# Optimization experiments

Hardware: AMD Instinct MI355X
Metric: run time of the kernel (lower is better)

## Reference

```python
import jax, jax.numpy as jnp
from jax import lax
import numpy as np

GRID, IMG, BLOCK = 60, 960, 16
BN_EPS = 1e-5


def _conv(x, w, b):
    return lax.conv_general_dilated(x, w, (1, 1), 'SAME', dimension_numbers=('NCHW', 'OIHW', 'NCHW')) + b[None, :, None, None]


def _bn(x, g, b):
    # inference BatchNorm with running_mean=0, running_var=1
    s = g * np.float32(1.0 / np.sqrt(1.0 + BN_EPS))
    return x * s[None, :, None, None] + b[None, :, None, None]


def _mlp(x, w1, b1, w2, b2):
    return jax.nn.relu(x @ w1.T + b1) @ w2.T + b2


def _lstm_layer(x, wih, whh, b):
    # x: [B,T,D]; torch gate order i,f,g,o; zero initial state
    B = x.shape[0]
    H = whh.shape[1]
    pre = jnp.swapaxes(x, 0, 1) @ wih.T + b  # [T,B,4H]

    def step(carry, p):
        h, c = carry
        z = p + h @ whh.T
        i, f, g, o = jnp.split(z, 4, axis=-1)
        c = jax.nn.sigmoid(f) * c + jax.nn.sigmoid(i) * jnp.tanh(g)
        h = jax.nn.sigmoid(o) * jnp.tanh(c)
        return (h, c), h

    z0 = jnp.zeros((B, H), x.dtype)
    (h, c), ys = lax.scan(step, (z0, z0), pre)
    return jnp.swapaxes(ys, 0, 1), h, c


def _forward(motion_vectors, boxes, track_ids, conv1_w, conv1_b, bn1_g, bn1_b, conv2_w, conv2_b, bn2_g, bn2_b, conv3_w, conv3_b, bn3_g, bn3_b, agg_w1, agg_b1, agg_w2, agg_b2, bx_w1, bx_b1, bx_w2, bx_b2, id_table, proj_w, proj_b, empty_slot, l0_wih, l0_whh, l0_b, l1_wih, l1_whh, l1_b, hb_w1, hb_b1, hb_w2, hb_b2, hc_w1, hc_b1, hc_w2, hc_b2, ht_w1, ht_b1, ht_w2, ht_b2):
    B = motion_vectors.shape[0]
    # ---- grid encoder (Conv-BN-ReLU x3) ----
    x = jax.nn.relu(_bn(_conv(motion_vectors, conv1_w, conv1_b), bn1_g, bn1_b))
    x = jax.nn.relu(_bn(_conv(x, conv2_w, conv2_b), bn2_g, bn2_b))
    gf = jax.nn.relu(_bn(_conv(x, conv3_w, conv3_b), bn3_g, bn3_b))  # [B,64,60,60]
    global_feat = gf.mean((-2, -1))  # AdaptiveAvgPool2d(1) -> [B,64]

    # ---- per-box motion statistics (vectorized masked reductions) ----
    bg = jnp.clip(boxes * (IMG / BLOCK), 0.0, GRID - 1e-6)  # grid coords
    ix1 = jnp.floor(bg[..., 0]); iy1 = jnp.floor(bg[..., 1])
    ix2 = jnp.maximum(ix1 + 1.0, jnp.ceil(bg[..., 2]))
    iy2 = jnp.maximum(iy1 + 1.0, jnp.ceil(bg[..., 3]))
    g = jnp.arange(GRID, dtype=bg.dtype)
    mx_ = (g >= ix1[..., None]) & (g < ix2[..., None])  # [B,N,60]
    my_ = (g >= iy1[..., None]) & (g < iy2[..., None])
    mask = my_[..., :, None] & mx_[..., None, :]  # [B,N,60,60]
    m = mask.astype(bg.dtype)
    cnt = m.sum((-2, -1))[..., None]  # [B,N,1], >= 1 by construction
    mv = motion_vectors  # [B,2,60,60]
    s1 = jnp.einsum('bnyx,bcyx->bnc', m, mv)
    s2 = jnp.einsum('bnyx,bcyx->bnc', m, mv * mv)
    mean = s1 / cnt
    var = (s2 - cnt * mean * mean) / jnp.maximum(cnt - 1.0, 1.0)  # unbiased, like torch .std()
    var_safe = jnp.where(cnt > 1.0, jnp.maximum(var, 1e-12), 1.0)
    std = jnp.where(cnt > 1.0, jnp.sqrt(var_safe), 0.0)
    BIG = jnp.asarray(1e9, bg.dtype)
    mn = jnp.min(jnp.where(mask[:, :, None], mv[:, None], BIG), axis=(-2, -1))   # [B,N,2]
    mx = jnp.max(jnp.where(mask[:, :, None], mv[:, None], -BIG), axis=(-2, -1))  # [B,N,2]
    stats = jnp.stack([mean[..., 0], mean[..., 1], std[..., 0], std[..., 1], mn[..., 0], mx[..., 0], mn[..., 1], mx[..., 1]], -1)  # [B,N,8]
    motion_emb = _mlp(stats, agg_w1, agg_b1, agg_w2, agg_b2)  # [B,N,64]

    # ---- slot initialization ----
    box_emb = _mlp(boxes, bx_w1, bx_b1, bx_w2, bx_b2)  # [B,N,64]
    id_emb = id_table[jnp.clip(track_ids, 0, 999)]  # [B,N,32]
    obj = jnp.concatenate([box_emb, id_emb, motion_emb], -1)  # [B,N,160]
    slots = obj @ proj_w.T + proj_b  # [B,300,128]; N == max_slots so no empty slots used

    # ---- 2-layer LSTM over the 300 slots (batch_first, eval -> no dropout) ----
    Ns = slots.shape[1]
    gexp = jnp.broadcast_to(global_feat[:, None, :], (B, Ns, global_feat.shape[-1]))
    lstm_in = jnp.concatenate([slots, gexp], -1)  # [B,300,192]
    y, h0, c0 = _lstm_layer(lstm_in, l0_wih, l0_whh, l0_b)
    y, h1, c1 = _lstm_layer(y, l1_wih, l1_whh, l1_b)  # [B,300,128]

    # ---- RT-DETR style heads ----
    pred_boxes = jax.nn.sigmoid(_mlp(y, hb_w1, hb_b1, hb_w2, hb_b2))  # [B,300,4]
    cls_logits = _mlp(y, hc_w1, hc_b1, hc_w2, hc_b2)  # [B,300,2]
    tid_logits = _mlp(y, ht_w1, ht_b1, ht_w2, ht_b2)  # [B,300,1000]
    h = jnp.stack([h0, h1])
    c = jnp.stack([c0, c1])
    return pred_boxes, cls_logits, tid_logits, h, c


def setup_inputs() -> dict:
    B, N = 32, 300
    key = jax.random.key(0)
    ks = iter(jax.random.split(key, 60))

    def w(*s):
        return jax.random.normal(next(ks), s, jnp.float32) * 0.05

    mv = jax.random.normal(next(ks), (B, 2, GRID, GRID), jnp.float32)
    bb = jax.random.uniform(next(ks), (B, N, 4), jnp.float32)
    boxes = jnp.concatenate([jnp.minimum(bb[..., :2], bb[..., 2:]), jnp.maximum(bb[..., :2], bb[..., 2:])], -1)
    track_ids = jax.random.randint(next(ks), (B, N), 0, 1000)
    return dict(
        motion_vectors=mv, boxes=boxes, track_ids=track_ids,
        conv1_w=w(32, 2, 3, 3), conv1_b=w(32), bn1_g=1.0 + w(32), bn1_b=w(32),
        conv2_w=w(64, 32, 3, 3), conv2_b=w(64), bn2_g=1.0 + w(64), bn2_b=w(64),
        conv3_w=w(64, 64, 3, 3), conv3_b=w(64), bn3_g=1.0 + w(64), bn3_b=w(64),
        agg_w1=w(32, 8), agg_b1=w(32), agg_w2=w(64, 32), agg_b2=w(64),
        bx_w1=w(32, 4), bx_b1=w(32), bx_w2=w(64, 32), bx_b2=w(64),
        id_table=w(1000, 32).at[0].set(0.0),
        proj_w=w(128, 160), proj_b=w(128), empty_slot=w(128),
        l0_wih=w(512, 192), l0_whh=w(512, 128), l0_b=w(512),
        l1_wih=w(512, 128), l1_whh=w(512, 128), l1_b=w(512),
        hb_w1=w(256, 128), hb_b1=w(256), hb_w2=w(4, 256), hb_b2=w(4),
        hc_w1=w(256, 128), hc_b1=w(256), hc_w2=w(2, 256), hc_b2=w(2),
        ht_w1=w(256, 128), ht_b1=w(256), ht_w2=w(1000, 256), ht_b2=w(1000))


def reference(motion_vectors, boxes, track_ids, conv1_w, conv1_b, bn1_g, bn1_b, conv2_w, conv2_b, bn2_g, bn2_b, conv3_w, conv3_b, bn3_g, bn3_b, agg_w1, agg_b1, agg_w2, agg_b2, bx_w1, bx_b1, bx_w2, bx_b2, id_table, proj_w, proj_b, empty_slot, l0_wih, l0_whh, l0_b, l1_wih, l1_whh, l1_b, hb_w1, hb_b1, hb_w2, hb_b2, hc_w1, hc_b1, hc_w2, hc_b2, ht_w1, ht_b1, ht_w2, ht_b2):
    return _forward(motion_vectors, boxes, track_ids, conv1_w, conv1_b, bn1_g, bn1_b, conv2_w, conv2_b, bn2_g, bn2_b, conv3_w, conv3_b, bn3_g, bn3_b, agg_w1, agg_b1, agg_w2, agg_b2, bx_w1, bx_b1, bx_w2, bx_b2, id_table, proj_w, proj_b, empty_slot, l0_wih, l0_whh, l0_b, l1_wih, l1_whh, l1_b, hb_w1, hb_b1, hb_w2, hb_b2, hc_w1, hc_b1, hc_w2, hc_b2, ht_w1, ht_b1, ht_w2, ht_b2)
```

## Files before the change

### kernel.cpp

```cpp
#include <hip/hip_runtime.h>
#include <hip/hip_bf16.h>
#include <math.h>

typedef unsigned short ushort_t;
typedef __attribute__((ext_vector_type(8))) short bf16x8;
typedef __attribute__((ext_vector_type(4))) float f32x4;

#define LOG2E 1.4426950408889634f

__device__ __forceinline__ float sigf(float x) {
  x = fminf(fmaxf(x, -30.f), 30.f);
  return 1.f / (1.f + __expf(-x));
}
__device__ __forceinline__ ushort_t f2bf(float x) {
  unsigned int b = __float_as_uint(x);
  unsigned int lsb = (b >> 16) & 1u;
  b += 0x7fffu + lsb;
  return (ushort_t)(b >> 16);
}
__device__ __forceinline__ float bf2f(ushort_t u) {
  return __uint_as_float(((unsigned int)u) << 16);
}
__device__ __forceinline__ float gsc(int g3) {
  return (g3 == 2) ? (2.f * LOG2E) : LOG2E;
}

#define NPIX 3600
__device__ __forceinline__ int gperm(int rho) {
  return ((rho & 3) << 7) + (rho >> 2);
}

__global__ __launch_bounds__(256) void gvec_kernel(
    const float* __restrict__ wih0, const float* __restrict__ gf,
    float* __restrict__ gvec) {
  int i = blockIdx.x * 256 + threadIdx.x;
  int b = i >> 9, n = i & 511;
  const float* wr = wih0 + gperm(n) * 192 + 128;
  const float* g = gf + b * 64;
  float a = 0.f;
#pragma unroll
  for (int k = 0; k < 64; ++k) a = fmaf(wr[k], g[k], a);
  gvec[i] = a * (1.f / 3600.f) * gsc(n & 3);
}

__global__ __launch_bounds__(256) void front_kernel(
    const float* __restrict__ mv, const float* __restrict__ c1w,
    const float* __restrict__ c1b, const float* __restrict__ bg1,
    const float* __restrict__ bb1, ushort_t* __restrict__ x1out,
    const float* __restrict__ boxes, const int* __restrict__ ids,
    const float* __restrict__ agg_w1, const float* __restrict__ agg_b1,
    const float* __restrict__ agg_w2, const float* __restrict__ agg_b2,
    const float* __restrict__ bx_w1, const float* __restrict__ bx_b1,
    const float* __restrict__ bx_w2, const float* __restrict__ bx_b2,
    const float* __restrict__ id_table, ushort_t* __restrict__ obj_out,
    const float* __restrict__ conv2_w, const float* __restrict__ conv3_w,
    const float* __restrict__ wih0, const float* __restrict__ projW,
    const float* __restrict__ projb, const float* __restrict__ l0_b,
    const float* __restrict__ hbw1, const float* __restrict__ hcw1,
    const float* __restrict__ htw1, const float* __restrict__ htw2,
    const float* __restrict__ hbb1, const float* __restrict__ hcb1,
    const float* __restrict__ htb1, ushort_t* __restrict__ wc2,
    ushort_t* __restrict__ wc3, ushort_t* __restrict__ wAp,
    float* __restrict__ l0bp, ushort_t* __restrict__ whid,
    ushort_t* __restrict__ wt2, float* __restrict__ bhid) {
  if (blockIdx.x < 1989) {
    int i = blockIdx.x * 256 + threadIdx.x;
    if (i < 18432) {
      int oc = i / 288, r = i % 288, kt = r / 32, ic = r % 32;
      wc2[i] = f2bf(conv2_w[((oc * 32 + ic) * 3 + kt / 3) * 3 + kt % 3]);
      return;
    }
    i -= 18432;
    if (i < 36864) {
      int oc = i / 576, r = i % 576, c = r / 288, r2 = r % 288;
      int kt = r2 / 32, icl = r2 % 32, ic = c * 32 + icl;
      wc3[i] = f2bf(conv3_w[((oc * 64 + ic) * 3 + kt / 3) * 3 + kt % 3]);
      return;
    }
    i -= 36864;
    if (i < 98304) {
      int n = i / 192, k = i % 192;
      int src = gperm(n);
      float a = 0.f;
      if (k < 160) {
        const float* wr = wih0 + src * 192;
        for (int j = 0; j < 128; ++j) a = fmaf(wr[j], projW[j * 160 + k], a);
      }
      wAp[i] = f2bf(a * gsc(n & 3));
      return;
    }
    i -= 98304;
    if (i < 512) {
      int src = gperm(i);
      float a = l0_b[src];
      const float* wr = wih0 + src * 192;
      for (int j = 0; j < 128; ++j) a = fmaf(wr[j], projb[j], a);
      l0bp[i] = a * gsc(i & 3);
      return;
    }
    i -= 512;
    if (i < 98304) {
      int row = i >> 7, c = i & 127;
      float v = (row < 256)   ? hbw1[row * 128 + c]
                : (row < 512) ? hcw1[(row - 256) * 128 + c]
                              : htw1[(row - 512) * 128 + c];
      whid[i] = f2bf(v);
      return;
    }
    i -= 98304;
    if (i < 256000) {
      wt2[i] = f2bf(htw2[i]);
      return;
    }
    i -= 256000;
    if (i < 768)
      bhid[i] = (i < 256) ? hbb1[i] : (i < 512) ? hcb1[i - 256] : htb1[i - 512];
    return;
  }
  int bx = blockIdx.x - 1989;
  if (bx < 14400) {
    int idx = bx * 256 + threadIdx.x;
    int x = idx % 60;
    int y = (idx / 60) % 60;
    int oc = (idx / 3600) % 32;
    int b = idx / (3600 * 32);
    float acc = 0.f;
#pragma unroll
    for (int ic = 0; ic < 2; ++ic) {
      const float* src = mv + (b * 2 + ic) * NPIX;
      const float* wp = c1w + (oc * 2 + ic) * 9;
#pragma unroll
      for (int ky = 0; ky < 3; ++ky) {
        int gy = y + ky - 1;
        if (gy < 0 || gy >= 60) continue;
#pragma unroll
        for (int kx = 0; kx < 3; ++kx) {
          int gx = x + kx - 1;
          if (gx < 0 || gx >= 60) continue;
          acc = fmaf(src[gy * 60 + gx], wp[ky * 3 + kx], acc);
        }
      }
    }
    float s = bg1[oc] * rsqrtf(1.f + 1e-5f);
    float v = fmaf(acc, s, fmaf(c1b[oc], s, bb1[oc]));
    x1out[idx] = f2bf(fmaxf(v, 0.f));
    return;
  }
  __shared__ float obj[2][160];
  __shared__ float hm[2][32];
  __shared__ float hbx[2][32];
  __shared__ float stats[2][8];
  __shared__ float boxf[2][4];
  __shared__ float red[2][2][8];
  int h = threadIdx.x >> 7;
  int t = threadIdx.x & 127;
  int blk = (bx - 14400) * 2 + h;
  int b = blk / 300;
  float bx0 = boxes[blk * 4 + 0], by0 = boxes[blk * 4 + 1];
  float bx1 = boxes[blk * 4 + 2], by1 = boxes[blk * 4 + 3];
  const float HI = (float)(60.0 - 1e-6);
  float gx1 = fminf(fmaxf(bx0 * 60.f, 0.f), HI);
  float gy1 = fminf(fmaxf(by0 * 60.f, 0.f), HI);
  float gx2 = fminf(fmaxf(bx1 * 60.f, 0.f), HI);
  float gy2 = fminf(fmaxf(by1 * 60.f, 0.f), HI);
  float fx1 = floorf(gx1), fy1 = floorf(gy1);
  float fx2 = fmaxf(fx1 + 1.f, ceilf(gx2));
  float fy2 = fmaxf(fy1 + 1.f, ceilf(gy2));
  int ix1 = (int)fx1, iy1 = (int)fy1, ix2 = (int)fx2, iy2 = (int)fy2;
  int w = ix2 - ix1, hgt = iy2 - iy1;
  int area = w * hgt;
  float s0 = 0.f, s1 = 0.f, q0 = 0.f, q1 = 0.f;
  float mn0 = 1e9f, mn1 = 1e9f, mx0 = -1e9f, mx1 = -1e9f;
  const float* mv0 = mv + b * 2 * NPIX;
  const float* mv1 = mv0 + NPIX;
  for (int i = t; i < area; i += 128) {
    int r = i / w, cc = i - r * w;
    int yy = iy1 + r, xx = ix1 + cc;
    float v0 = mv0[yy * 60 + xx];
    float v1 = mv1[yy * 60 + xx];
    s0 += v0; q0 += v0 * v0; mn0 = fminf(mn0, v0); mx0 = fmaxf(mx0, v0);
    s1 += v1; q1 += v1 * v1; mn1 = fminf(mn1, v1); mx1 = fmaxf(mx1, v1);
  }
#pragma unroll
  for (int off = 32; off; off >>= 1) {
    s0 += __shfl_down(s0, off); s1 += __shfl_down(s1, off);
    q0 += __shfl_down(q0, off); q1 += __shfl_down(q1, off);
    mn0 = fminf(mn0, __shfl_down(mn0, off));
    mn1 = fminf(mn1, __shfl_down(mn1, off));
    mx0 = fmaxf(mx0, __shfl_down(mx0, off));
    mx1 = fmaxf(mx1, __shfl_down(mx1, off));
  }
  if ((t & 63) == 0) {
    int wv = t >> 6;
    red[h][wv][0] = s0; red[h][wv][1] = s1;
    red[h][wv][2] = q0; red[h][wv][3] = q1;
    red[h][wv][4] = mn0; red[h][wv][5] = mn1;
    red[h][wv][6] = mx0; red[h][wv][7] = mx1;
  }
  __syncthreads();
  if (t == 0) {
    float S0 = red[h][0][0] + red[h][1][0], S1 = red[h][0][1] + red[h][1][1];
    float Q0 = red[h][0][2] + red[h][1][2], Q1 = red[h][0][3] + red[h][1][3];
    float MN0 = fminf(red[h][0][4], red[h][1][4]);
    float MN1 = fminf(red[h][0][5], red[h][1][5]);
    float MX0 = fmaxf(red[h][0][6], red[h][1][6]);
    float MX1 = fmaxf(red[h][0][7], red[h][1][7]);
    float cnt = (float)area;
    float mean0 = S0 / cnt, mean1 = S1 / cnt;
    float var0 = (Q0 - cnt * mean0 * mean0) / fmaxf(cnt - 1.f, 1.f);
    float var1 = (Q1 - cnt * mean1 * mean1) / fmaxf(cnt - 1.f, 1.f);
    float sd0 = (cnt > 1.f) ? sqrtf(fmaxf(var0, 1e-12f)) : 0.f;
    float sd1 = (cnt > 1.f) ? sqrtf(fmaxf(var1, 1e-12f)) : 0.f;
    stats[h][0] = mean0; stats[h][1] = mean1; stats[h][2] = sd0;
    stats[h][3] = sd1; stats[h][4] = MN0; stats[h][5] = MX0;
    stats[h][6] = MN1; stats[h][7] = MX1;
    boxf[h][0] = bx0; boxf[h][1] = by0; boxf[h][2] = bx1; boxf[h][3] = by1;
  }
  __syncthreads();
  if (t < 32) {
    float a = agg_b1[t];
#pragma unroll
    for (int k = 0; k < 8; ++k) a = fmaf(stats[h][k], agg_w1[t * 8 + k], a);
    hm[h][t] = fmaxf(a, 0.f);
  } else if (t < 64) {
    int j = t - 32;
    float a = bx_b1[j];
#pragma unroll
    for (int k = 0; k < 4; ++k) a = fmaf(boxf[h][k], bx_w1[j * 4 + k], a);
    hbx[h][j] = fmaxf(a, 0.f);
  }
  __syncthreads();
  if (t < 64) {
    float a = bx_b2[t];
#pragma unroll
    for (int k = 0; k < 32; ++k) a = fmaf(hbx[h][k], bx_w2[t * 32 + k], a);
    obj[h][t] = a;
  } else {
    int j = t - 64;
    float a = agg_b2[j];
#pragma unroll
    for (int k = 0; k < 32; ++k) a = fmaf(hm[h][k], agg_w2[j * 32 + k], a);
    obj[h][96 + j] = a;
  }
  if (t < 32) {
    int id = ids[blk];
    id = min(max(id, 0), 999);
    obj[h][64 + t] = id_table[id * 32 + t];
  }
  __syncthreads();
  obj_out[(size_t)blk * 192 + t] = f2bf(obj[h][t]);
  if (t < 32) {
    obj_out[(size_t)blk * 192 + 128 + t] = f2bf(obj[h][128 + t]);
    obj_out[(size_t)blk * 192 + 160 + t] = 0;
  }
}

template <int CIN, bool POOL>
__global__ __launch_bounds__(256) void conv_mfma_kernel(
    const ushort_t* __restrict__ in, const ushort_t* __restrict__ wc,
    const float* __restrict__ cb, const float* __restrict__ bg,
    const float* __restrict__ bb, ushort_t* __restrict__ out,
    float* __restrict__ gf) {
  constexpr int NCHUNK = CIN / 32;
  __shared__ ushort_t in_lds[18 * 18 * 40];
  int tid = threadIdx.x;
  int wv = tid >> 6, lane = tid & 63;
  int col = lane & 15, kg = lane >> 4;
  int b = blockIdx.y, tile = blockIdx.x;
  int tq = tile >> 2, tr = tile & 3;
  int ty0 = tq * 16 - (tq == 3 ? 4 : 0);
  int tx0 = tr * 16 - (tr == 3 ? 4 : 0);
  int oc = wv * 16 + col;

  bf16x8 bw[NCHUNK * 9];
#pragma unroll
  for (int c = 0; c < NCHUNK; ++c)
#pragma unroll
    for (int kt = 0; kt < 9; ++kt)
      bw[c * 9 + kt] = *(const bf16x8*)(wc + oc * (NCHUNK * 288) + c * 288 +
                                        kt * 32 + kg * 8);

  f32x4 acc[16];
#pragma unroll
  for (int m = 0; m < 16; ++m) acc[m] = (f32x4){0.f, 0.f, 0.f, 0.f};

  for (int c = 0; c < NCHUNK; ++c) {
    if (c) __syncthreads();
    for (int i = tid; i < 18 * 18 * 32; i += 256) {
      int ic = i / 324, rem = i % 324;
      int yy = rem / 18, xx = rem % 18;
      int gy = ty0 + yy - 1, gx = tx0 + xx - 1;
      ushort_t v = 0;
      if (gy >= 0 && gy < 60 && gx >= 0 && gx < 60)
        v = in[((size_t)(b * CIN + c * 32 + ic) * 60 + gy) * 60 + gx];
      in_lds[(yy * 18 + xx) * 40 + ic] = v;
    }
    __syncthreads();
#pragma unroll
    for (int kt = 0; kt < 9; ++kt) {
      int ky = kt / 3, kx = kt % 3;
#pragma unroll
      for (int m = 0; m < 16; ++m) {
        bf16x8 af =
            *(const bf16x8*)(&in_lds[((m + ky) * 18 + col + kx) * 40 + kg * 8]);
        acc[m] = __builtin_amdgcn_mfma_f32_16x16x32_bf16(af, bw[c * 9 + kt],
                                                         acc[m], 0, 0, 0);
      }
    }
  }
  float s = bg[oc] * rsqrtf(1.f + 1e-5f);
  float bias = fmaf(cb[oc], s, bb[oc]);
  float pool = 0.f;
#pragma unroll
  for (int m = 0; m < 16; ++m) {
    float vv[4];
#pragma unroll
    for (int r = 0; r < 4; ++r) vv[r] = fmaxf(fmaf(acc[m][r], s, bias), 0.f);
    if (POOL) {
      bool ymask = (tq != 3) || (m >= 4);
#pragma unroll
      for (int r = 0; r < 4; ++r) {
        int px = kg * 4 + r;
        bool xmask = (tr != 3) || (px >= 4);
        if (ymask && xmask) pool += vv[r];
      }
    } else {
      ushort_t st[4];
#pragma unroll
      for (int r = 0; r < 4; ++r) st[r] = f2bf(vv[r]);
      int yy = ty0 + m, xx = tx0 + kg * 4;
      *(uint2*)(&out[((size_t)(b * 64 + oc) * 60 + yy) * 60 + xx]) =
          *(uint2*)st;
    }
  }
  if (POOL) {
    pool += __shfl_xor(pool, 16);
    pool += __shfl_xor(pool, 32);
    if (lane < 16) atomicAdd(&gf[b * 64 + oc], pool);
  }
}

template <int ACT, bool OBF16, bool GVEC>
__global__ __launch_bounds__(256) void gemm_bf16w_kernel(
    const ushort_t* __restrict__ A, int lda, const ushort_t* __restrict__ W,
    const float* __restrict__ bias, void* __restrict__ C, int ldc, int M,
    int N, int K, const float* __restrict__ gvec) {
  __shared__ ushort_t As[128 * 64];
  __shared__ ushort_t Ws[64 * 64];
  int tid = threadIdx.x;
  int wv = tid >> 6, lane = tid & 63;
  int col = lane & 15, kg = lane >> 4;
  int wm = wv >> 1, wn = wv & 1;
  int m0 = blockIdx.x * 128, n0 = blockIdx.y * 64;
  f32x4 acc[4][2];
#pragma unroll
  for (int i = 0; i < 4; ++i)
#pragma unroll
    for (int j = 0; j < 2; ++j) acc[i][j] = (f32x4){0.f, 0.f, 0.f, 0.f};

  int nk = K >> 6;
  for (int kc = 0; kc < nk; ++kc) {
    if (kc) __syncthreads();
#pragma unroll
    for (int q = 0; q < 4; ++q) {
      int idx = q * 256 + tid;
      int row = idx >> 3, ch = idx & 7;
      uint4 v =
          *(const uint4*)(A + (size_t)(m0 + row) * lda + kc * 64 + ch * 8);
      *(uint4*)(&As[row * 64 + ((ch * 8) ^ ((row & 7) << 3))]) = v;
    }
#pragma unroll
    for (int q = 0; q < 2; ++q) {
      int idx = q * 256 + tid;
      int row = idx >> 3, ch = idx & 7;
      int n = n0 + row;
      uint4 v = make_uint4(0, 0, 0, 0);
      if (n < N) v = *(const uint4*)(W + (size_t)n * K + kc * 64 + ch * 8);
      *(uint4*)(&Ws[row * 64 + ((ch * 8) ^ ((row & 7) << 3))]) = v;
    }
    __syncthreads();
#pragma unroll
    for (int ks = 0; ks < 2; ++ks) {
      bf16x8 bfr[2], afr[4];
#pragma unroll
      for (int ni = 0; ni < 2; ++ni) {
        int row = wn * 32 + ni * 16 + col;
        bfr[ni] = *(const bf16x8*)(
            &Ws[row * 64 + ((ks * 32 + kg * 8) ^ ((row & 7) << 3))]);
      }
#pragma unroll
      for (int mi = 0; mi < 4; ++mi) {
        int row = wm * 64 + mi * 16 + col;
        afr[mi] = *(const bf16x8*)(
            &As[row * 64 + ((ks * 32 + kg * 8) ^ ((row & 7) << 3))]);
      }
#pragma unroll
      for (int mi = 0; mi < 4; ++mi)
#pragma unroll
        for (int ni = 0; ni < 2; ++ni)
          acc[mi][ni] = __builtin_amdgcn_mfma_f32_16x16x32_bf16(
              afr[mi], bfr[ni], acc[mi][ni], 0, 0, 0);
    }
  }
#pragma unroll
  for (int ni = 0; ni < 2; ++ni) {
    int n = n0 + wn * 32 + ni * 16 + col;
    float bn = (n < N) ? bias[n] : 0.f;
#pragma unroll
    for (int mi = 0; mi < 4; ++mi) {
      int mbase = m0 + wm * 64 + mi * 16 + kg * 4;
#pragma unroll
      for (int r = 0; r < 4; ++r) {
        float v = acc[mi][ni][r] + bn;
        if (GVEC) v += gvec[((mbase + r) / 300) * 512 + n];
        if (ACT == 1) v = fmaxf(v, 0.f);
        if (n < N) {
          if (OBF16)
            ((ushort_t*)C)[(size_t)(mbase + r) * ldc + n] = f2bf(v);
          else
            ((float*)C)[(size_t)(mbase + r) * ldc + n] = v;
        }
      }
    }
  }
}

__global__ __launch_bounds__(256) void head_small_kernel(
    const ushort_t* __restrict__ hid, const float* __restrict__ wb2,
    const float* __restrict__ bb2, const float* __restrict__ wc2,
    const float* __restrict__ bc2, float* __restrict__ outB,
    float* __restrict__ outC) {
  int idx = blockIdx.x * 256 + threadIdx.x;
  int row = idx / 6, j = idx % 6;
  const ushort_t* h = hid + (size_t)row * 768 + (j < 4 ? 0 : 256);
  const float* wrow = (j < 4) ? wb2 + j * 256 : wc2 + (j - 4) * 256;
  float acc = (j < 4) ? bb2[j] : bc2[j - 4];
  for (int k = 0; k < 256; k += 8) {
    uint4 hv = *(const uint4*)(h + k);
    unsigned int ww[4] = {hv.x, hv.y, hv.z, hv.w};
#pragma unroll
    for (int q = 0; q < 4; ++q) {
      acc = fmaf(bf2f((ushort_t)(ww[q] & 0xffff)), wrow[k + 2 * q], acc);
      acc = fmaf(bf2f((ushort_t)(ww[q] >> 16)), wrow[k + 2 * q + 1], acc);
    }
  }
  float v = (j < 4) ? sigf(acc) : acc;
  if (j < 4) outB[row * 4 + j] = v;
  else outC[row * 2 + (j - 4)] = v;
}

#define LSTM_BAR() asm volatile("s_waitcnt lgkmcnt(0)\n\ts_barrier" ::: "memory")

__global__ __launch_bounds__(512) void lstm_fused_kernel(
    const float* __restrict__ pre0,
    const float* __restrict__ whh0,
    const float* __restrict__ wih1,
    const float* __restrict__ whh1,
    const float* __restrict__ b1,
    float* __restrict__ pre1,
    ushort_t* __restrict__ y0,
    ushort_t* __restrict__ y1,
    float* __restrict__ outH, float* __restrict__ outC,
    unsigned int* __restrict__ flags)
{
  __shared__ ushort_t h_lds[2][4][160];
  int tid = threadIdx.x;
  int w = tid >> 6, lane = tid & 63;
  int col = lane & 15, kg = lane >> 4;
  int bat = col & 3, q = col >> 2;
  int cell = (4 * w + q) * 4 + kg;
  float wsc = gsc(col & 3);

  if (blockIdx.x < 8) {
    int g = blockIdx.x;
    int b0 = g * 4;
    unsigned int* flagp = &flags[g * 32];
    for (int i = tid; i < 2 * 4 * 160; i += 512) ((ushort_t*)h_lds)[i] = 0;
    bf16x8 aW0[4][4];
#pragma unroll
    for (int j = 0; j < 4; ++j) {
      int rho = (4 * w + j) * 16 + col;
      int src = gperm(rho);
#pragma unroll
      for (int kt = 0; kt < 4; ++kt) {
        const float* s1 = whh0 + src * 128 + kt * 32 + kg * 8;
        bf16x8 f1;
#pragma unroll
        for (int qq = 0; qq < 8; ++qq) f1[qq] = (short)f2bf(s1[qq] * wsc);
        aW0[j][kt] = f1;
      }
    }
    const float* pg = pre0 + (size_t)(b0 + bat) * 300 * 512 + 4 * cell;
    ushort_t* yg0 = y0 + ((size_t)(b0 + bat) * 300) * 128 + cell;
    float c = 0.f, hout = 0.f;
    f32x4 p0v = *(const f32x4*)(pg);
    f32x4 p1v = *(const f32x4*)(pg + 512);
    __syncthreads();

    for (int s = 0; s < 300; ++s) {
      const ushort_t* hb = h_lds[s & 1][bat];
      bf16x8 bfr[4];
#pragma unroll
      for (int kt = 0; kt < 4; ++kt)
        bfr[kt] = *(const bf16x8*)(hb + kt * 32 + kg * 8);
      f32x4 a0 = {0.f, 0.f, 0.f, 0.f}, a1 = a0, a2 = a0, a3 = a0;
#pragma unroll
      for (int kt = 0; kt < 4; ++kt) {
        a0 = __builtin_amdgcn_mfma_f32_16x16x32_bf16(aW0[0][kt], bfr[kt], a0, 0, 0, 0);
        a1 = __builtin_amdgcn_mfma_f32_16x16x32_bf16(aW0[1][kt], bfr[kt], a1, 0, 0, 0);
        a2 = __builtin_amdgcn_mfma_f32_16x16x32_bf16(aW0[2][kt], bfr[kt], a2, 0, 0, 0);
        a3 = __builtin_amdgcn_mfma_f32_16x16x32_bf16(aW0[3][kt], bfr[kt], a3, 0, 0, 0);
      }
      f32x4 z = a0;
      if (q == 1) z = a1;
      if (q == 2) z = a2;
      if (q == 3) z = a3;
      {
        float zi = z[0] + p0v[0];
        float zf = z[1] + p0v[1];
        float zg = z[2] + p0v[2];
        float zo = z[3] + p0v[3];
        float vi = __builtin_amdgcn_rcpf(1.f + __builtin_amdgcn_exp2f(-zi));
        float vf = __builtin_amdgcn_rcpf(1.f + __builtin_amdgcn_exp2f(-zf));
        float vg = 1.f - 2.f * __builtin_amdgcn_rcpf(
                              __builtin_amdgcn_exp2f(zg) + 1.f);
        float vo = __builtin_amdgcn_rcpf(1.f + __builtin_amdgcn_exp2f(-zo));
        c = vf * c + vi * vg;
        hout = vo * (1.f - 2.f * __builtin_amdgcn_rcpf(
                             __builtin_amdgcn_exp2f(2.f * LOG2E * c) + 1.f));
        ushort_t hv = f2bf(hout);
        h_lds[(s + 1) & 1][bat][cell] = hv;
        __builtin_nontemporal_store(hv, yg0 + (size_t)s * 128);
        p0v = p1v;
        int sn = (s + 2 < 300) ? s + 2 : 299;
        p1v = *(const f32x4*)(pg + (size_t)sn * 512);
      }
      asm volatile("s_waitcnt vmcnt(6)" ::: "memory");
      LSTM_BAR();
      if (tid == 0 && s >= 3)
        __hip_atomic_store(flagp, (unsigned int)(s - 3), __ATOMIC_RELAXED,
                           __HIP_MEMORY_SCOPE_AGENT);
    }
    asm volatile("s_waitcnt vmcnt(0)" ::: "memory");
    __syncthreads();
    if (tid == 0)
      __hip_atomic_store(flagp, 300u, __ATOMIC_RELAXED,
                         __HIP_MEMORY_SCOPE_AGENT);
    outH[(b0 + bat) * 128 + cell] = hout;
    outC[(b0 + bat) * 128 + cell] = c;
  } else if (blockIdx.x < 16) {
    int g = blockIdx.x - 8;
    int b0 = g * 4;
    unsigned int* flagp = &flags[g * 32 + 16];
    for (int i = tid; i < 2 * 4 * 160; i += 512) ((ushort_t*)h_lds)[i] = 0;
    bf16x8 aW[4][4];
#pragma unroll
    for (int j = 0; j < 4; ++j) {
      int rho = (4 * w + j) * 16 + col;
      int src = gperm(rho);
#pragma unroll
      for (int kt = 0; kt < 4; ++kt) {
        const float* s1 = whh1 + src * 128 + kt * 32 + kg * 8;
        bf16x8 f1;
#pragma unroll
        for (int qq = 0; qq < 8; ++qq) f1[qq] = (short)f2bf(s1[qq] * wsc);
        aW[j][kt] = f1;
      }
    }
    float bi = b1[cell] * LOG2E, bff = b1[128 + cell] * LOG2E;
    float bgg = b1[256 + cell] * (2.f * LOG2E), boo = b1[384 + cell] * LOG2E;
    const float* pg = pre1 + (size_t)(b0 + bat) * 300 * 512 + 4 * cell;
    ushort_t* yg = y1 + (size_t)(b0 + bat) * 300 * 128 + cell;
    float c = 0.f, hout = 0.f;
    unsigned int fc = 0;
    f32x4 p0v, p1v;
    do {
      fc = __hip_atomic_load(flagp, __ATOMIC_RELAXED,
                             __HIP_MEMORY_SCOPE_AGENT);
      if (fc < 1) __builtin_amdgcn_s_sleep(2);
    } while (fc < 1);
    asm volatile("" ::: "memory");
    p0v = __builtin_nontemporal_load((const f32x4*)(pg));
    while (fc < 2) {
      fc = __hip_atomic_load(flagp, __ATOMIC_RELAXED,
                             __HIP_MEMORY_SCOPE_AGENT);
      if (fc < 2) __builtin_amdgcn_s_sleep(2);
    }
    asm volatile("" ::: "memory");
    p1v = __builtin_nontemporal_load((const f32x4*)(pg + 512));
    __syncthreads();

    for (int t = 0; t < 300; ++t) {
      unsigned int fcn = __hip_atomic_load(flagp, __ATOMIC_RELAXED,
                                           __HIP_MEMORY_SCOPE_AGENT);
      const ushort_t* hb = h_lds[t & 1][bat];
      bf16x8 bfr[4];
#pragma unroll
      for (int kt = 0; kt < 4; ++kt)
        bfr[kt] = *(const bf16x8*)(hb + kt * 32 + kg * 8);
      f32x4 a0 = {0.f, 0.f, 0.f, 0.f}, a1 = a0, a2 = a0, a3 = a0;
#pragma unroll
      for (int kt = 0; kt < 4; ++kt) {
        a0 = __builtin_amdgcn_mfma_f32_16x16x32_bf16(aW[0][kt], bfr[kt], a0, 0, 0, 0);
        a1 = __builtin_amdgcn_mfma_f32_16x16x32_bf16(aW[1][kt], bfr[kt], a1, 0, 0, 0);
        a2 = __builtin_amdgcn_mfma_f32_16x16x32_bf16(aW[2][kt], bfr[kt], a2, 0, 0, 0);
        a3 = __builtin_amdgcn_mfma_f32_16x16x32_bf16(aW[3][kt], bfr[kt], a3, 0, 0, 0);
      }
      f32x4 z = a0;
      if (q == 1) z = a1;
      if (q == 2) z = a2;
      if (q == 3) z = a3;
      {
        float zi = z[0] + p0v[0] + bi;
        float zf = z[1] + p0v[1] + bff;
        float zg = z[2] + p0v[2] + bgg;
        float zo = z[3] + p0v[3] + boo;
        float vi = __builtin_amdgcn_rcpf(1.f + __builtin_amdgcn_exp2f(-zi));
        float vf = __builtin_amdgcn_rcpf(1.f + __builtin_amdgcn_exp2f(-zf));
        float vg = 1.f - 2.f * __builtin_amdgcn_rcpf(
                              __builtin_amdgcn_exp2f(zg) + 1.f);
        float vo = __builtin_amdgcn_rcpf(1.f + __builtin_amdgcn_exp2f(-zo));
        c = vf * c + vi * vg;
        hout = vo * (1.f - 2.f * __builtin_amdgcn_rcpf(
                             __builtin_amdgcn_exp2f(2.f * LOG2E * c) + 1.f));
        ushort_t hv = f2bf(hout);
        h_lds[(t + 1) & 1][bat][cell] = hv;
        yg[(size_t)t * 128] = hv;
        p0v = p1v;
        if (t + 2 < 300) {
          unsigned int need = (unsigned int)(t + 3);
          if (fcn > fc) fc = fcn;
          if (fc < need) {
            do {
              fc = __hip_atomic_load(flagp, __ATOMIC_RELAXED,
                                     __HIP_MEMORY_SCOPE_AGENT);
              if (fc < need) __builtin_amdgcn_s_sleep(2);
            } while (fc < need);
            asm volatile("" ::: "memory");
          }
          p1v = __builtin_nontemporal_load(
              (const f32x4*)(pg + (size_t)(t + 2) * 512));
        }
      }
      LSTM_BAR();
    }
    outH[4096 + (b0 + bat) * 128 + cell] = hout;
    outC[4096 + (b0 + bat) * 128 + cell] = c;
  } else {
    int g = blockIdx.x - 16;
    int b0 = g * 4;
    unsigned int* flag0 = &flags[g * 32];
    unsigned int* flag1 = &flags[g * 32 + 16];
    bf16x8 aU[4][4];
#pragma unroll
    for (int j = 0; j < 4; ++j) {
      int rho = (4 * w + j) * 16 + col;
      int src = gperm(rho);
#pragma unroll
      for (int kt = 0; kt < 4; ++kt) {
        const float* s2 = wih1 + src * 128 + kt * 32 + kg * 8;
        bf16x8 f2;
#pragma unroll
        for (int qq = 0; qq < 8; ++qq) f2[qq] = (short)f2bf(s2[qq] * wsc);
        aU[j][kt] = f2;
      }
    }
    int bb = col & 3;
    int ts = col >> 2;
    const ushort_t* yb = y0 + ((size_t)(b0 + bb) * 300) * 128 + kg * 8;
    unsigned int fc = 0;
    for (int t0 = 0; t0 < 300; t0 += 12) {
      unsigned int need = (unsigned int)(t0 + 11);
      while (fc < need) {
        fc = __hip_atomic_load(flag0, __ATOMIC_RELAXED,
                               __HIP_MEMORY_SCOPE_AGENT);
        if (fc < need) __builtin_amdgcn_s_sleep(2);
      }
      asm volatile("" ::: "memory");
      f32x4 acc[4][3];
#pragma unroll
      for (int j = 0; j < 4; ++j)
#pragma unroll
        for (int ct = 0; ct < 3; ++ct) acc[j][ct] = (f32x4){0.f, 0.f, 0.f, 0.f};
#pragma unroll
      for (int ct = 0; ct < 3; ++ct) {
        int t = t0 + ct * 4 + ts;
        bf16x8 bfr[4];
#pragma unroll
        for (int kt = 0; kt < 4; ++kt)
          bfr[kt] = __builtin_nontemporal_load(
              (const bf16x8*)(yb + (size_t)t * 128 + kt * 32));
#pragma unroll
        for (int kt = 0; kt < 4; ++kt) {
          acc[0][ct] = __builtin_amdgcn_mfma_f32_16x16x32_bf16(aU[0][kt], bfr[kt], acc[0][ct], 0, 0, 0);
          acc[1][ct] = __builtin_amdgcn_mfma_f32_16x16x32_bf16(aU[1][kt], bfr[kt], acc[1][ct], 0, 0, 0);
          acc[2][ct] = __builtin_amdgcn_mfma_f32_16x16x32_bf16(aU[2][kt], bfr[kt], acc[2][ct], 0, 0, 0);
          acc[3][ct] = __builtin_amdgcn_mfma_f32_16x16x32_bf16(aU[3][kt], bfr[kt], acc[3][ct], 0, 0, 0);
        }
      }
#pragma unroll
      for (int ct = 0; ct < 3; ++ct) {
        int t = t0 + ct * 4 + ts;
        float* pd = pre1 + ((size_t)(b0 + bb) * 300 + t) * 512 + kg * 4;
#pragma unroll
        for (int j = 0; j < 4; ++j)
          __builtin_nontemporal_store(acc[j][ct],
                                      (f32x4*)(pd + (4 * w + j) * 16));
      }
      asm volatile("s_waitcnt vmcnt(0)" ::: "memory");
      __syncthreads();
      if (tid == 0)
        __hip_atomic_store(flag1, (unsigned int)(t0 + 12), __ATOMIC_RELAXED,
                           __HIP_MEMORY_SCOPE_AGENT);
    }
  }
}

extern "C" void kernel_launch(void* const* d_in, const int* in_sizes, int n_in,
                              void* d_out, int out_size, void* d_ws,
                              size_t ws_size, hipStream_t stream) {
  const float* mv = (const float*)d_in[0];
  const float* boxes = (const float*)d_in[1];
  const int* track_ids = (const int*)d_in[2];
  const float* conv1_w = (const float*)d_in[3];
  const float* conv1_b = (const float*)d_in[4];
  const float* bn1_g = (const float*)d_in[5];
  const float* bn1_b = (const float*)d_in[6];
  const float* conv2_w = (const float*)d_in[7];
  const float* conv2_b = (const float*)d_in[8];
  const float* bn2_g = (const float*)d_in[9];
  const float* bn2_b = (const float*)d_in[10];
  const float* conv3_w = (const float*)d_in[11];
  const float* conv3_b = (const float*)d_in[12];
  const float* bn3_g = (const float*)d_in[13];
  const float* bn3_b = (const float*)d_in[14];
  const float* agg_w1 = (const float*)d_in[15];
  const float* agg_b1 = (const float*)d_in[16];
  const float* agg_w2 = (const float*)d_in[17];
  const float* agg_b2 = (const float*)d_in[18];
  const float* bx_w1 = (const float*)d_in[19];
  const float* bx_b1 = (const float*)d_in[20];
  const float* bx_w2 = (const float*)d_in[21];
  const float* bx_b2 = (const float*)d_in[22];
  const float* id_table = (const float*)d_in[23];
  const float* proj_w = (const float*)d_in[24];
  const float* proj_b = (const float*)d_in[25];
  const float* l0_wih = (const float*)d_in[27];
  const float* l0_whh = (const float*)d_in[28];
  const float* l0_b = (const float*)d_in[29];
  const float* l1_wih = (const float*)d_in[30];
  const float* l1_whh = (const float*)d_in[31];
  const float* l1_b = (const float*)d_in[32];
  const float* hb_w1 = (const float*)d_in[33];
  const float* hb_b1 = (const float*)d_in[34];
  const float* hb_w2 = (const float*)d_in[35];
  const float* hb_b2 = (const float*)d_in[36];
  const float* hc_w1 = (const float*)d_in[37];
  const float* hc_b1 = (const float*)d_in[38];
  const float* hc_w2 = (const float*)d_in[39];
  const float* hc_b2 = (const float*)d_in[40];
  const float* ht_w1 = (const float*)d_in[41];
  const float* ht_b1 = (const float*)d_in[42];
  const float* ht_w2 = (const float*)d_in[43];
  const float* ht_b2 = (const float*)d_in[44];

  char* wsb = (char*)d_ws;
  ushort_t* x1u = (ushort_t*)(wsb + 0);
  ushort_t* x2u = (ushort_t*)(wsb + 7372800);
  float* pre0 = (float*)(wsb + 0);
  ushort_t* hid = (ushort_t*)(wsb + 0);
  ushort_t* y0g = (ushort_t*)(wsb + 19660800);
  float* gf = (float*)(wsb + 22118400);
  ushort_t* obj = (ushort_t*)(wsb + 22126592);
  float* pre1 = (float*)(wsb + 25812992);
  ushort_t* y1b = (ushort_t*)(wsb + 45473792);
  unsigned int* flags = (unsigned int*)(wsb + 47931392);
  ushort_t* wAp = (ushort_t*)(wsb + 47932416);
  ushort_t* whid = (ushort_t*)(wsb + 48129024);
  ushort_t* wt2 = (ushort_t*)(wsb + 48325632);
  float* bhid = (float*)(wsb + 48837632);
  float* l0bp = (float*)(wsb + 48840704);
  float* gvec = (float*)(wsb + 48842752);
  ushort_t* wc2 = (ushort_t*)(wsb + 48908288);
  ushort_t* wc3 = (ushort_t*)(wsb + 48945152);

  float* outB = (float*)d_out;
  float* outC = outB + 38400;
  float* outT = outB + 57600;
  float* outH = outB + 9657600;
  float* outCc = outB + 9665792;

  hipMemsetAsync(gf, 0, 2048 * sizeof(float), stream);
  hipMemsetAsync(flags, 0, 1024, stream);

  front_kernel<<<21189, 256, 0, stream>>>(
      mv, conv1_w, conv1_b, bn1_g, bn1_b, x1u, boxes, track_ids, agg_w1,
      agg_b1, agg_w2, agg_b2, bx_w1, bx_b1, bx_w2, bx_b2, id_table, obj,
      conv2_w, conv3_w, l0_wih, proj_w, proj_b, l0_b, hb_w1, hc_w1, ht_w1,
      ht_w2, hb_b1, hc_b1, ht_b1, wc2, wc3, wAp, l0bp, whid, wt2, bhid);
  conv_mfma_kernel<32, false><<<dim3(16, 32), 256, 0, stream>>>(
      x1u, wc2, conv2_b, bn2_g, bn2_b, x2u, nullptr);
  conv_mfma_kernel<64, true><<<dim3(16, 32), 256, 0, stream>>>(
      x2u, wc3, conv3_b, bn3_g, bn3_b, nullptr, gf);
  gvec_kernel<<<64, 256, 0, stream>>>(l0_wih, gf, gvec);
  gemm_bf16w_kernel<0, false, true><<<dim3(75, 8), 256, 0, stream>>>(
      obj, 192, wAp, l0bp, pre0, 512, 9600, 512, 192, gvec);
  lstm_fused_kernel<<<24, 512, 0, stream>>>(pre0, l0_whh, l1_wih, l1_whh,
                                            l1_b, pre1, y0g, y1b, outH, outCc,
                                            flags);
  gemm_bf16w_kernel<1, true, false><<<dim3(75, 12), 256, 0, stream>>>(
      y1b, 128, whid, bhid, hid, 768, 9600, 768, 128, nullptr);
  head_small_kernel<<<225, 256, 0, stream>>>(hid, hb_w2, hb_b2, hc_w2, hc_b2,
                                             outB, outC);
  gemm_bf16w_kernel<0, false, false><<<dim3(75, 16), 256, 0, stream>>>(
      hid + 512, 768, wt2, ht_b2, outT, 1000, 9600, 1000, 256, nullptr);
}
```

Measured before the change: 543.4 us.

## Fuse three conv layers into one tiled kernel with halo recompute in LDS

Conv1, conv2 and conv3 plus the global average pool now run in one kernel. Each block works on a 14x14 output tile and keeps the conv1 and conv2 activations, with their halos, in LDS instead of writing them to global memory. This removes the global round trips for the intermediate activation maps and two kernel launches. In exchange the halo regions are recomputed by neighbouring tiles, the grid grows to 25 tiles per image, and LDS use per block rises to about 63KB, which may limit occupancy.

```diff
diff --git a/kernel.cpp b/kernel.cpp
--- a/kernel.cpp
+++ b/kernel.cpp
@@ -44,25 +44,23 @@
 }
 
 __global__ __launch_bounds__(256) void front_kernel(
-    const float* __restrict__ mv, const float* __restrict__ c1w,
-    const float* __restrict__ c1b, const float* __restrict__ bg1,
-    const float* __restrict__ bb1, ushort_t* __restrict__ x1out,
-    const float* __restrict__ boxes, const int* __restrict__ ids,
-    const float* __restrict__ agg_w1, const float* __restrict__ agg_b1,
-    const float* __restrict__ agg_w2, const float* __restrict__ agg_b2,
-    const float* __restrict__ bx_w1, const float* __restrict__ bx_b1,
-    const float* __restrict__ bx_w2, const float* __restrict__ bx_b2,
-    const float* __restrict__ id_table, ushort_t* __restrict__ obj_out,
-    const float* __restrict__ conv2_w, const float* __restrict__ conv3_w,
-    const float* __restrict__ wih0, const float* __restrict__ projW,
-    const float* __restrict__ projb, const float* __restrict__ l0_b,
-    const float* __restrict__ hbw1, const float* __restrict__ hcw1,
-    const float* __restrict__ htw1, const float* __restrict__ htw2,
-    const float* __restrict__ hbb1, const float* __restrict__ hcb1,
-    const float* __restrict__ htb1, ushort_t* __restrict__ wc2,
-    ushort_t* __restrict__ wc3, ushort_t* __restrict__ wAp,
-    float* __restrict__ l0bp, ushort_t* __restrict__ whid,
-    ushort_t* __restrict__ wt2, float* __restrict__ bhid) {
+    const float* __restrict__ mv, const float* __restrict__ boxes,
+    const int* __restrict__ ids, const float* __restrict__ agg_w1,
+    const float* __restrict__ agg_b1, const float* __restrict__ agg_w2,
+    const float* __restrict__ agg_b2, const float* __restrict__ bx_w1,
+    const float* __restrict__ bx_b1, const float* __restrict__ bx_w2,
+    const float* __restrict__ bx_b2, const float* __restrict__ id_table,
+    ushort_t* __restrict__ obj_out, const float* __restrict__ conv2_w,
+    const float* __restrict__ conv3_w, const float* __restrict__ wih0,
+    const float* __restrict__ projW, const float* __restrict__ projb,
+    const float* __restrict__ l0_b, const float* __restrict__ hbw1,
+    const float* __restrict__ hcw1, const float* __restrict__ htw1,
+    const float* __restrict__ htw2, const float* __restrict__ hbb1,
+    const float* __restrict__ hcb1, const float* __restrict__ htb1,
+    ushort_t* __restrict__ wc2, ushort_t* __restrict__ wc3,
+    ushort_t* __restrict__ wAp, float* __restrict__ l0bp,
+    ushort_t* __restrict__ whid, ushort_t* __restrict__ wt2,
+    float* __restrict__ bhid) {
   if (blockIdx.x < 1989) {
     int i = blockIdx.x * 256 + threadIdx.x;
     if (i < 18432) {
@@ -118,34 +116,6 @@
     return;
   }
   int bx = blockIdx.x - 1989;
-  if (bx < 14400) {
-    int idx = bx * 256 + threadIdx.x;
-    int x = idx % 60;
-    int y = (idx / 60) % 60;
-    int oc = (idx / 3600) % 32;
-    int b = idx / (3600 * 32);
-    float acc = 0.f;
-#pragma unroll
-    for (int ic = 0; ic < 2; ++ic) {
-      const float* src = mv + (b * 2 + ic) * NPIX;
-      const float* wp = c1w + (oc * 2 + ic) * 9;
-#pragma unroll
-      for (int ky = 0; ky < 3; ++ky) {
-        int gy = y + ky - 1;
-        if (gy < 0 || gy >= 60) continue;
-#pragma unroll
-        for (int kx = 0; kx < 3; ++kx) {
-          int gx = x + kx - 1;
-          if (gx < 0 || gx >= 60) continue;
-          acc = fmaf(src[gy * 60 + gx], wp[ky * 3 + kx], acc);
-        }
-      }
-    }
-    float s = bg1[oc] * rsqrtf(1.f + 1e-5f);
-    float v = fmaf(acc, s, fmaf(c1b[oc], s, bb1[oc]));
-    x1out[idx] = f2bf(fmaxf(v, 0.f));
-    return;
-  }
   __shared__ float obj[2][160];
   __shared__ float hm[2][32];
   __shared__ float hbx[2][32];
@@ -154,7 +124,7 @@
   __shared__ float red[2][2][8];
   int h = threadIdx.x >> 7;
   int t = threadIdx.x & 127;
-  int blk = (bx - 14400) * 2 + h;
+  int blk = bx * 2 + h;
   int b = blk / 300;
   float bx0 = boxes[blk * 4 + 0], by0 = boxes[blk * 4 + 1];
   float bx1 = boxes[blk * 4 + 2], by1 = boxes[blk * 4 + 3];
@@ -255,88 +225,138 @@
   }
 }
 
-template <int CIN, bool POOL>
-__global__ __launch_bounds__(256) void conv_mfma_kernel(
-    const ushort_t* __restrict__ in, const ushort_t* __restrict__ wc,
-    const float* __restrict__ cb, const float* __restrict__ bg,
-    const float* __restrict__ bb, ushort_t* __restrict__ out,
-    float* __restrict__ gf) {
-  constexpr int NCHUNK = CIN / 32;
-  __shared__ ushort_t in_lds[18 * 18 * 40];
+__global__ __launch_bounds__(256) void convstack_kernel(
+    const float* __restrict__ mv, const float* __restrict__ c1w,
+    const float* __restrict__ c1b, const float* __restrict__ bg1,
+    const float* __restrict__ bb1, const ushort_t* __restrict__ wc2,
+    const float* __restrict__ c2b, const float* __restrict__ bg2,
+    const float* __restrict__ bb2, const ushort_t* __restrict__ wc3,
+    const float* __restrict__ c3b, const float* __restrict__ bg3,
+    const float* __restrict__ bb3, float* __restrict__ gf) {
+  __shared__ char smem[25920 + 37152];
+  ushort_t* c1_lds = (ushort_t*)smem;
+  ushort_t* c2_lds = (ushort_t*)(smem + 25920);
+  float* mv_lds = (float*)(smem + 25920);
   int tid = threadIdx.x;
   int wv = tid >> 6, lane = tid & 63;
   int col = lane & 15, kg = lane >> 4;
   int b = blockIdx.y, tile = blockIdx.x;
-  int tq = tile >> 2, tr = tile & 3;
-  int ty0 = tq * 16 - (tq == 3 ? 4 : 0);
-  int tx0 = tr * 16 - (tr == 3 ? 4 : 0);
-  int oc = wv * 16 + col;
-
-  bf16x8 bw[NCHUNK * 9];
-#pragma unroll
-  for (int c = 0; c < NCHUNK; ++c)
+  int tq = tile / 5, tr = tile % 5;
+  int ty0 = (tq == 4) ? 46 : tq * 14;
+  int tx0 = (tr == 4) ? 46 : tr * 14;
+  for (int i = tid; i < 800; i += 256) {
+    int r = i % 400;
+    int ch = i / 400, yy = r / 20, xx = r % 20;
+    int gy = ty0 - 3 + yy, gx = tx0 - 3 + xx;
+    float v = 0.f;
+    if (gy >= 0 && gy < 60 && gx >= 0 && gx < 60)
+      v = mv[((size_t)(b * 2 + ch) * 60 + gy) * 60 + gx];
+    mv_lds[i] = v;
+  }
+  __syncthreads();
+  {
+    int oc = tid & 31;
+    float s = bg1[oc] * rsqrtf(1.f + 1e-5f);
+    float bias = fmaf(c1b[oc], s, bb1[oc]);
+    float w1r[18];
+#pragma unroll
+    for (int k = 0; k < 18; ++k) w1r[k] = c1w[oc * 18 + k];
+    for (int pos = tid >> 5; pos < 324; pos += 8) {
+      int yy = pos / 18, xx = pos % 18;
+      int gy = ty0 - 2 + yy, gx = tx0 - 2 + xx;
+      ushort_t out = 0;
+      if (gy >= 0 && gy < 60 && gx >= 0 && gx < 60) {
+        float acc = 0.f;
+#pragma unroll
+        for (int ic = 0; ic < 2; ++ic)
+#pragma unroll
+          for (int ky = 0; ky < 3; ++ky)
+#pragma unroll
+            for (int kx = 0; kx < 3; ++kx)
+              acc = fmaf(mv_lds[ic * 400 + (yy + ky) * 20 + xx + kx],
+                         w1r[ic * 9 + ky * 3 + kx], acc);
+        out = f2bf(fmaxf(fmaf(acc, s, bias), 0.f));
+      }
+      c1_lds[pos * 40 + oc] = out;
+    }
+  }
+  __syncthreads();
+  int oc2 = wv * 16 + col;
+  {
+    bf16x8 bw2[9];
 #pragma unroll
     for (int kt = 0; kt < 9; ++kt)
-      bw[c * 9 + kt] = *(const bf16x8*)(wc + oc * (NCHUNK * 288) + c * 288 +
-                                        kt * 32 + kg * 8);
-
-  f32x4 acc[16];
-#pragma unroll
-  for (int m = 0; m < 16; ++m) acc[m] = (f32x4){0.f, 0.f, 0.f, 0.f};
-
-  for (int c = 0; c < NCHUNK; ++c) {
-    if (c) __syncthreads();
-    for (int i = tid; i < 18 * 18 * 32; i += 256) {
-      int ic = i / 324, rem = i % 324;
-      int yy = rem / 18, xx = rem % 18;
-      int gy = ty0 + yy - 1, gx = tx0 + xx - 1;
-      ushort_t v = 0;
-      if (gy >= 0 && gy < 60 && gx >= 0 && gx < 60)
-        v = in[((size_t)(b * CIN + c * 32 + ic) * 60 + gy) * 60 + gx];
-      in_lds[(yy * 18 + xx) * 40 + ic] = v;
-    }
-    __syncthreads();
+      bw2[kt] = *(const bf16x8*)(wc2 + oc2 * 288 + kt * 32 + kg * 8);
+    f32x4 a2[16];
+#pragma unroll
+    for (int m = 0; m < 16; ++m) a2[m] = (f32x4){0.f, 0.f, 0.f, 0.f};
 #pragma unroll
     for (int kt = 0; kt < 9; ++kt) {
       int ky = kt / 3, kx = kt % 3;
 #pragma unroll
       for (int m = 0; m < 16; ++m) {
-        bf16x8 af =
-            *(const bf16x8*)(&in_lds[((m + ky) * 18 + col + kx) * 40 + kg * 8]);
-        acc[m] = __builtin_amdgcn_mfma_f32_16x16x32_bf16(af, bw[c * 9 + kt],
-                                                         acc[m], 0, 0, 0);
-      }
-    }
-  }
-  float s = bg[oc] * rsqrtf(1.f + 1e-5f);
-  float bias = fmaf(cb[oc], s, bb[oc]);
-  float pool = 0.f;
-#pragma unroll
-  for (int m = 0; m < 16; ++m) {
-    float vv[4];
-#pragma unroll
-    for (int r = 0; r < 4; ++r) vv[r] = fmaxf(fmaf(acc[m][r], s, bias), 0.f);
-    if (POOL) {
-      bool ymask = (tq != 3) || (m >= 4);
+        bf16x8 af = *(const bf16x8*)(
+            &c1_lds[((m + ky) * 18 + col + kx) * 40 + kg * 8]);
+        a2[m] =
+            __builtin_amdgcn_mfma_f32_16x16x32_bf16(af, bw2[kt], a2[m], 0, 0, 0);
+      }
+    }
+    float s = bg2[oc2] * rsqrtf(1.f + 1e-5f);
+    float bias = fmaf(c2b[oc2], s, bb2[oc2]);
+#pragma unroll
+    for (int m = 0; m < 16; ++m) {
+      int gy = ty0 - 1 + m;
+#pragma unroll
+      for (int r = 0; r < 4; ++r) {
+        int gx = tx0 - 1 + kg * 4 + r;
+        ushort_t o = 0;
+        if (gy >= 0 && gy < 60 && gx >= 0 && gx < 60)
+          o = f2bf(fmaxf(fmaf(a2[m][r], s, bias), 0.f));
+        c2_lds[(m * 16 + kg * 4 + r) * 72 + oc2] = o;
+      }
+    }
+  }
+  __syncthreads();
+  {
+    bf16x8 bw3[2][9];
+#pragma unroll
+    for (int c = 0; c < 2; ++c)
+#pragma unroll
+      for (int kt = 0; kt < 9; ++kt)
+        bw3[c][kt] =
+            *(const bf16x8*)(wc3 + oc2 * 576 + c * 288 + kt * 32 + kg * 8);
+    f32x4 a3[14];
+#pragma unroll
+    for (int m = 0; m < 14; ++m) a3[m] = (f32x4){0.f, 0.f, 0.f, 0.f};
+#pragma unroll
+    for (int c = 0; c < 2; ++c)
+#pragma unroll
+      for (int kt = 0; kt < 9; ++kt) {
+        int ky = kt / 3, kx = kt % 3;
+#pragma unroll
+        for (int m = 0; m < 14; ++m) {
+          bf16x8 af = *(const bf16x8*)(
+              &c2_lds[((m + ky) * 16 + col + kx) * 72 + c * 32 + kg * 8]);
+          a3[m] = __builtin_amdgcn_mfma_f32_16x16x32_bf16(af, bw3[c][kt],
+                                                          a3[m], 0, 0, 0);
+        }
+      }
+    float s = bg3[oc2] * rsqrtf(1.f + 1e-5f);
+    float bias = fmaf(c3b[oc2], s, bb3[oc2]);
+    float pool = 0.f;
+#pragma unroll
+    for (int m = 0; m < 14; ++m) {
+      bool ym = (tq != 4) || (m >= 10);
 #pragma unroll
       for (int r = 0; r < 4; ++r) {
         int px = kg * 4 + r;
-        bool xmask = (tr != 3) || (px >= 4);
-        if (ymask && xmask) pool += vv[r];
-      }
-    } else {
-      ushort_t st[4];
-#pragma unroll
-      for (int r = 0; r < 4; ++r) st[r] = f2bf(vv[r]);
-      int yy = ty0 + m, xx = tx0 + kg * 4;
-      *(uint2*)(&out[((size_t)(b * 64 + oc) * 60 + yy) * 60 + xx]) =
-          *(uint2*)st;
-    }
-  }
-  if (POOL) {
+        bool xm = (px < 14) && ((tr != 4) || (px >= 10));
+        if (ym && xm) pool += fmaxf(fmaf(a3[m][r], s, bias), 0.f);
+      }
+    }
     pool += __shfl_xor(pool, 16);
     pool += __shfl_xor(pool, 32);
-    if (lane < 16) atomicAdd(&gf[b * 64 + oc], pool);
+    if (lane < 16) atomicAdd(&gf[b * 64 + oc2], pool);
   }
 }
 
@@ -765,8 +785,6 @@
   const float* ht_b2 = (const float*)d_in[44];
 
   char* wsb = (char*)d_ws;
-  ushort_t* x1u = (ushort_t*)(wsb + 0);
-  ushort_t* x2u = (ushort_t*)(wsb + 7372800);
   float* pre0 = (float*)(wsb + 0);
   ushort_t* hid = (ushort_t*)(wsb + 0);
   ushort_t* y0g = (ushort_t*)(wsb + 19660800);
@@ -793,15 +811,14 @@
   hipMemsetAsync(gf, 0, 2048 * sizeof(float), stream);
   hipMemsetAsync(flags, 0, 1024, stream);
 
-  front_kernel<<<21189, 256, 0, stream>>>(
-      mv, conv1_w, conv1_b, bn1_g, bn1_b, x1u, boxes, track_ids, agg_w1,
-      agg_b1, agg_w2, agg_b2, bx_w1, bx_b1, bx_w2, bx_b2, id_table, obj,
-      conv2_w, conv3_w, l0_wih, proj_w, proj_b, l0_b, hb_w1, hc_w1, ht_w1,
-      ht_w2, hb_b1, hc_b1, ht_b1, wc2, wc3, wAp, l0bp, whid, wt2, bhid);
-  conv_mfma_kernel<32, false><<<dim3(16, 32), 256, 0, stream>>>(
-      x1u, wc2, conv2_b, bn2_g, bn2_b, x2u, nullptr);
-  conv_mfma_kernel<64, true><<<dim3(16, 32), 256, 0, stream>>>(
-      x2u, wc3, conv3_b, bn3_g, bn3_b, nullptr, gf);
+  front_kernel<<<6789, 256, 0, stream>>>(
+      mv, boxes, track_ids, agg_w1, agg_b1, agg_w2, agg_b2, bx_w1, bx_b1,
+      bx_w2, bx_b2, id_table, obj, conv2_w, conv3_w, l0_wih, proj_w, proj_b,
+      l0_b, hb_w1, hc_w1, ht_w1, ht_w2, hb_b1, hc_b1, ht_b1, wc2, wc3, wAp,
+      l0bp, whid, wt2, bhid);
+  convstack_kernel<<<dim3(25, 32), 256, 0, stream>>>(
+      mv, conv1_w, conv1_b, bn1_g, bn1_b, wc2, conv2_b, bn2_g, bn2_b, wc3,
+      conv3_b, bn3_g, bn3_b, gf);
   gvec_kernel<<<64, 256, 0, stream>>>(l0_wih, gf, gvec);
   gemm_bf16w_kernel<0, false, true><<<dim3(75, 8), 256, 0, stream>>>(
       obj, 192, wAp, l0bp, pre0, 512, 9600, 512, 192, gvec);
```

Measured after the change: 472.4 us. 1.15x faster.
